# Performance work log

Hardware: AMD Instinct MI355X
Metric: run time of the kernel (lower is better)

## Reference

```python
import jax, jax.numpy as jnp
import numpy as np

N_NODES = 100000


def _degrees(src, dst, n):
    ones = jnp.ones(src.shape[0], dtype=jnp.float32)
    deg_out = jax.ops.segment_sum(ones, src, num_segments=n)
    deg_in = jax.ops.segment_sum(ones, dst, num_segments=n)
    # DGL clamps degrees to min 1 before pow(-0.5)
    return jnp.clip(deg_out, 1.0) ** -0.5, jnp.clip(deg_in, 1.0) ** -0.5


def _graph_conv(x, src, dst, W, b, norm_out, norm_in, n):
    # norm='both': scale source by D_out^-1/2, aggregate (copy_u + sum), scale dest by D_in^-1/2
    # weight applied before aggregation (in_feats >= out_feats for all layers; math-equivalent)
    h = (x * norm_out[:, None]) @ W                      # [N, out]
    agg = jax.ops.segment_sum(h[src], dst, num_segments=n)  # SpMM via gather+scatter-add
    return agg * norm_in[:, None] + b


def setup_inputs() -> dict:
    key = jax.random.key(0)
    ks = jax.random.split(key, 8)
    E = 1600000
    return {
        "in_feat": jax.random.normal(ks[0], (N_NODES, 128), dtype=jnp.float32),
        "src": jax.random.randint(ks[1], (E,), 0, N_NODES),
        "dst": jax.random.randint(ks[2], (E,), 0, N_NODES),
        "W1": jax.random.normal(ks[3], (128, 128), dtype=jnp.float32) * (128 ** -0.5),
        "b1": jnp.zeros((128,), dtype=jnp.float32),
        "W2": jax.random.normal(ks[4], (128, 128), dtype=jnp.float32) * (128 ** -0.5),
        "b2": jnp.zeros((128,), dtype=jnp.float32),
        "W3": jax.random.normal(ks[5], (128, 64), dtype=jnp.float32) * (128 ** -0.5),
        "b3": jnp.zeros((64,), dtype=jnp.float32),
    }


def reference(in_feat, src, dst, W1, b1, W2, b2, W3, b3):
    n = in_feat.shape[0]
    norm_out, norm_in = _degrees(src, dst, n)
    h = jax.nn.relu(_graph_conv(in_feat, src, dst, W1, b1, norm_out, norm_in, n))
    h = jax.nn.relu(_graph_conv(h, src, dst, W2, b2, norm_out, norm_in, n))
    h = _graph_conv(h, src, dst, W3, b3, norm_out, norm_in, n)
    return h
```

## Files before the change

kernel.cpp:

```cpp
#include <hip/hip_runtime.h>

#define THREADS 256
#define SCAN_BLK 1024
#define NR 8
#define NC 32
#define RSTRIDE 12544

typedef __attribute__((ext_vector_type(8))) short short8;
typedef __attribute__((ext_vector_type(4))) float floatx4;

__device__ __forceinline__ ushort f2bf(float f) {
    union { float f; uint u; } v; v.f = f;
    uint u = v.u;
    return (ushort)((u + 0x7FFFu + ((u >> 16) & 1u)) >> 16);
}
__device__ __forceinline__ float bf_lo(uint u) {
    union { uint u; float f; } v; v.u = u << 16; return v.f;
}
__device__ __forceinline__ float bf_hi(uint u) {
    union { uint u; float f; } v; v.u = u & 0xFFFF0000u; return v.f;
}

__global__ __launch_bounds__(256) void hist_out_kernel(const int* __restrict__ src,
                                                       int* __restrict__ cnt_out,
                                                       int n, int E) {
    __shared__ uint cnt[RSTRIDE];
    const int range = blockIdx.x % NR;
    const int chunk = blockIdx.x / NR;
    const int Rsz = (n + NR - 1) / NR;
    const int lo  = range * Rsz;
    const int R   = min(n - lo, Rsz);
    if (R <= 0) return;
    for (int i = threadIdx.x; i < R; i += THREADS) cnt[i] = 0;
    __syncthreads();
    const int per = (E + NC - 1) / NC;
    const int c0 = chunk * per;
    const int c1 = min(E, c0 + per);
    int i = c0 + threadIdx.x * 4;
    for (; i + 4 <= c1; i += THREADS * 4) {
        int4 v = *(const int4*)(src + i);
        if ((unsigned)(v.x - lo) < (unsigned)R) atomicAdd(&cnt[v.x - lo], 1u);
        if ((unsigned)(v.y - lo) < (unsigned)R) atomicAdd(&cnt[v.y - lo], 1u);
        if ((unsigned)(v.z - lo) < (unsigned)R) atomicAdd(&cnt[v.z - lo], 1u);
        if ((unsigned)(v.w - lo) < (unsigned)R) atomicAdd(&cnt[v.w - lo], 1u);
    }
    if (i < c1) {
        for (int e = i; e < c1 && e < i + 4; ++e) {
            int s = src[e];
            if ((unsigned)(s - lo) < (unsigned)R) atomicAdd(&cnt[s - lo], 1u);
        }
    }
    __syncthreads();
    for (int k = threadIdx.x; k < R; k += THREADS) {
        uint c = cnt[k];
        if (c) atomicAdd(&cnt_out[lo + k], (int)c);
    }
}

__global__ __launch_bounds__(256) void csr_phaseA(const int* __restrict__ dst,
                                                  ushort* __restrict__ PC, int n, int E) {
    __shared__ uint cnt[RSTRIDE / 2];
    const int range = blockIdx.x % NR;
    const int chunk = blockIdx.x / NR;
    const int Rsz = (n + NR - 1) / NR;
    const int lo  = range * Rsz;
    const int R   = min(n - lo, Rsz);
    if (R <= 0) return;
    const int Rp = (R + 2) >> 1;
    for (int i = threadIdx.x; i < Rp; i += THREADS) cnt[i] = 0;
    __syncthreads();
    const int per = (E + NC - 1) / NC;
    const int c0 = chunk * per;
    const int c1 = min(E, c0 + per);
    int i = c0 + threadIdx.x * 4;
    for (; i + 4 <= c1; i += THREADS * 4) {
        int4 v = *(const int4*)(dst + i);
        int kx = v.x - lo, ky = v.y - lo, kz = v.z - lo, kw = v.w - lo;
        if ((unsigned)kx < (unsigned)R) atomicAdd(&cnt[kx >> 1], (kx & 1) ? 65536u : 1u);
        if ((unsigned)ky < (unsigned)R) atomicAdd(&cnt[ky >> 1], (ky & 1) ? 65536u : 1u);
        if ((unsigned)kz < (unsigned)R) atomicAdd(&cnt[kz >> 1], (kz & 1) ? 65536u : 1u);
        if ((unsigned)kw < (unsigned)R) atomicAdd(&cnt[kw >> 1], (kw & 1) ? 65536u : 1u);
    }
    if (i < c1) {
        for (int e = i; e < c1 && e < i + 4; ++e) {
            int k = dst[e] - lo;
            if ((unsigned)k < (unsigned)R) atomicAdd(&cnt[k >> 1], (k & 1) ? 65536u : 1u);
        }
    }
    __syncthreads();
    ushort* pc = PC + (size_t)(range * NC + chunk) * RSTRIDE;
    for (int k = threadIdx.x; k < R; k += THREADS) {
        uint c = cnt[k >> 1];
        pc[k] = (ushort)((k & 1) ? (c >> 16) : (c & 0xFFFFu));
    }
}

__global__ void csr_colsum(const ushort* __restrict__ PC, int* __restrict__ cnt_in, int n) {
    int gk = blockIdx.x * blockDim.x + threadIdx.x;
    if (gk >= n) return;
    const int Rsz = (n + NR - 1) / NR;
    int r = gk / Rsz, k = gk - r * Rsz;
    int t = 0;
    #pragma unroll 4
    for (int c = 0; c < NC; ++c)
        t += PC[(size_t)(r * NC + c) * RSTRIDE + k];
    cnt_in[gk] = t;
}

__global__ void csr_mkbase(const ushort* __restrict__ PC, const int* __restrict__ row_off,
                           int* __restrict__ B, int n) {
    int gk = blockIdx.x * blockDim.x + threadIdx.x;
    if (gk >= n) return;
    const int Rsz = (n + NR - 1) / NR;
    int r = gk / Rsz, k = gk - r * Rsz;
    int base = row_off[gk];
    for (int c = 0; c < NC; ++c) {
        size_t idx = (size_t)(r * NC + c) * RSTRIDE + k;
        B[idx] = base;
        base += PC[idx];
    }
}

__global__ __launch_bounds__(256) void csr_phaseC(const int* __restrict__ src,
                                                  const int* __restrict__ dst,
                                                  const int* __restrict__ B,
                                                  int* __restrict__ csr_src, int n, int E) {
    __shared__ int cur[RSTRIDE];
    const int range = blockIdx.x % NR;
    const int chunk = blockIdx.x / NR;
    const int Rsz = (n + NR - 1) / NR;
    const int lo  = range * Rsz;
    const int R   = min(n - lo, Rsz);
    if (R <= 0) return;
    const int* b = B + (size_t)(range * NC + chunk) * RSTRIDE;
    for (int i = threadIdx.x; i < R; i += THREADS) cur[i] = b[i];
    __syncthreads();
    const int per = (E + NC - 1) / NC;
    const int c0 = chunk * per;
    const int c1 = min(E, c0 + per);
    int i = c0 + threadIdx.x * 4;
    for (; i + 4 <= c1; i += THREADS * 4) {
        int4 d = *(const int4*)(dst + i);
        int4 s = *(const int4*)(src + i);
        int kx = d.x - lo, ky = d.y - lo, kz = d.z - lo, kw = d.w - lo;
        if ((unsigned)kx < (unsigned)R) csr_src[atomicAdd(&cur[kx], 1)] = s.x;
        if ((unsigned)ky < (unsigned)R) csr_src[atomicAdd(&cur[ky], 1)] = s.y;
        if ((unsigned)kz < (unsigned)R) csr_src[atomicAdd(&cur[kz], 1)] = s.z;
        if ((unsigned)kw < (unsigned)R) csr_src[atomicAdd(&cur[kw], 1)] = s.w;
    }
    if (i < c1) {
        for (int e = i; e < c1 && e < i + 4; ++e) {
            int k = dst[e] - lo;
            if ((unsigned)k < (unsigned)R) csr_src[atomicAdd(&cur[k], 1)] = src[e];
        }
    }
}

__global__ void scan_phase1(const int* __restrict__ cnt, int* __restrict__ blk_sums, int n) {
    int base = blockIdx.x * SCAN_BLK;
    int t = threadIdx.x;
    int sum = 0;
    for (int i = t; i < SCAN_BLK; i += THREADS) {
        int idx = base + i;
        sum += (idx < n) ? cnt[idx] : 0;
    }
    __shared__ int wsum[4];
    for (int off = 32; off > 0; off >>= 1) sum += __shfl_down(sum, off);
    if ((t & 63) == 0) wsum[t >> 6] = sum;
    __syncthreads();
    if (t == 0) blk_sums[blockIdx.x] = wsum[0] + wsum[1] + wsum[2] + wsum[3];
}

__global__ void scan_phase2(int* __restrict__ blk_sums, int nb) {
    __shared__ int s[1024];
    int t = threadIdx.x;
    s[t] = (t < nb) ? blk_sums[t] : 0;
    __syncthreads();
    for (int off = 1; off < 1024; off <<= 1) {
        int v = s[t];
        if (t >= off) v += s[t - off];
        __syncthreads();
        s[t] = v;
        __syncthreads();
    }
    if (t < nb) blk_sums[t] = (t == 0) ? 0 : s[t - 1];
}

__global__ void scan_phase3(const int* __restrict__ cnt, const int* __restrict__ cnt_out,
                            const int* __restrict__ blk_sums,
                            int* __restrict__ row_off, float* __restrict__ norm_in,
                            float* __restrict__ norm_out, int n, int E) {
    __shared__ int ts[THREADS];
    int b = blockIdx.x, t = threadIdx.x;
    int base = b * SCAN_BLK + t * 4;
    int local[4], val[4]; int s = 0;
    #pragma unroll
    for (int k = 0; k < 4; ++k) {
        local[k] = s;
        int idx = base + k;
        int v = (idx < n) ? cnt[idx] : 0;
        val[k] = v;
        s += v;
    }
    ts[t] = s;
    __syncthreads();
    for (int off = 1; off < THREADS; off <<= 1) {
        int v = ts[t];
        if (t >= off) v += ts[t - off];
        __syncthreads();
        ts[t] = v;
        __syncthreads();
    }
    int excl = (t == 0) ? 0 : ts[t - 1];
    int boff = blk_sums[b];
    #pragma unroll
    for (int k = 0; k < 4; ++k) {
        int idx = base + k;
        if (idx < n) {
            row_off[idx] = boff + excl + local[k];
            norm_in[idx]  = rsqrtf((float)max(val[k], 1));
            norm_out[idx] = rsqrtf((float)max(cnt_out[idx], 1));
        }
    }
    if (b == 0 && t == 0) row_off[n] = E;
}

__device__ __forceinline__ void wpack_one(const float* __restrict__ W, ushort* __restrict__ Wpk,
                                          int OUT, int t) {
    int lane = t & 63, kk = (t >> 6) & 3, ct = t >> 8;
    int col = ct * 16 + (lane & 15);
    int k0 = kk * 32 + (lane >> 4) * 8;
    #pragma unroll
    for (int j = 0; j < 8; ++j)
        Wpk[t * 8 + j] = f2bf(W[(size_t)(k0 + j) * OUT + col]);
}

__global__ void wpack_all(const float* __restrict__ W1, const float* __restrict__ W2,
                          const float* __restrict__ W3, ushort* __restrict__ Wpk1,
                          ushort* __restrict__ Wpk2, ushort* __restrict__ Wpk3) {
    int t = blockIdx.x * blockDim.x + threadIdx.x;
    if (t < 2048)      wpack_one(W1, Wpk1, 128, t);
    else if (t < 4096) wpack_one(W2, Wpk2, 128, t - 2048);
    else if (t < 5120) wpack_one(W3, Wpk3, 64,  t - 4096);
}

template<int OUT, bool IN_F32>
__global__ __launch_bounds__(256) void mfma_gemm(const void* __restrict__ xv,
                                                 const ushort* __restrict__ Wpk,
                                                 const float* __restrict__ norm,
                                                 ushort* __restrict__ h, int n) {
    __shared__ ushort xs[64 * 136];
    const int t = threadIdx.x;
    const int row0 = blockIdx.x * 64;

    if (IN_F32) {
        const float* x = (const float*)xv;
        #pragma unroll
        for (int i = 0; i < 8; ++i) {
            int e = (i * 256 + t) * 4;
            int row = e >> 7, col = e & 127;
            int gr = min(row0 + row, n - 1);
            float nf = norm[gr];
            float4 v = *(const float4*)(x + (size_t)gr * 128 + col);
            ushort4 p;
            p.x = f2bf(v.x * nf); p.y = f2bf(v.y * nf);
            p.z = f2bf(v.z * nf); p.w = f2bf(v.w * nf);
            *(ushort4*)(&xs[row * 136 + col]) = p;
        }
    } else {
        const ushort* x = (const ushort*)xv;
        #pragma unroll
        for (int i = 0; i < 4; ++i) {
            int e = (i * 256 + t) * 8;
            int row = e >> 7, col = e & 127;
            int gr = min(row0 + row, n - 1);
            float nf = norm[gr];
            uint4 v = *(const uint4*)(x + (size_t)gr * 128 + col);
            uint4 o;
            o.x = f2bf(bf_lo(v.x) * nf) | ((uint)f2bf(bf_hi(v.x) * nf) << 16);
            o.y = f2bf(bf_lo(v.y) * nf) | ((uint)f2bf(bf_hi(v.y) * nf) << 16);
            o.z = f2bf(bf_lo(v.z) * nf) | ((uint)f2bf(bf_hi(v.z) * nf) << 16);
            o.w = f2bf(bf_lo(v.w) * nf) | ((uint)f2bf(bf_hi(v.w) * nf) << 16);
            *(uint4*)(&xs[row * 136 + col]) = o;
        }
    }
    __syncthreads();

    const int wave = t >> 6, lane = t & 63;
    const int r = lane & 15, g = lane >> 4;
    const int nrow0 = row0 + wave * 16;

    short8 a[4];
    #pragma unroll
    for (int kk = 0; kk < 4; ++kk)
        a[kk] = *(const short8*)(&xs[(wave * 16 + r) * 136 + kk * 32 + g * 8]);

    const short8* wp = (const short8*)Wpk;
    #pragma unroll
    for (int ct = 0; ct < OUT / 16; ++ct) {
        floatx4 acc = {0.f, 0.f, 0.f, 0.f};
        #pragma unroll
        for (int kk = 0; kk < 4; ++kk) {
            short8 b = wp[(ct * 4 + kk) * 64 + lane];
            acc = __builtin_amdgcn_mfma_f32_16x16x32_bf16(a[kk], b, acc, 0, 0, 0);
        }
        int col = ct * 16 + r;
        #pragma unroll
        for (int rr = 0; rr < 4; ++rr) {
            int grow = nrow0 + g * 4 + rr;
            if (grow < n) h[(size_t)grow * OUT + col] = f2bf(acc[rr]);
        }
    }
}

template<bool RELU>
__global__ __launch_bounds__(256) void agg128(const ushort* __restrict__ h,
                                              const int* __restrict__ row_off,
                                              const int* __restrict__ csr_src,
                                              const float* __restrict__ nin,
                                              const float* __restrict__ bias,
                                              ushort* __restrict__ out, int n) {
    const int wave = threadIdx.x >> 6;
    const int lane = threadIdx.x & 63;
    const uint* hu = (const uint*)h;
    for (int node = blockIdx.x * 4 + wave; node < n; node += gridDim.x * 4) {
        int beg = row_off[node], end = row_off[node + 1];
        float a0 = 0.f, a1 = 0.f;
        int j = beg;
        for (; j + 3 < end; j += 4) {
            int s0 = csr_src[j], s1 = csr_src[j + 1], s2 = csr_src[j + 2], s3 = csr_src[j + 3];
            uint u0 = hu[(size_t)s0 * 64 + lane];
            uint u1 = hu[(size_t)s1 * 64 + lane];
            uint u2 = hu[(size_t)s2 * 64 + lane];
            uint u3 = hu[(size_t)s3 * 64 + lane];
            a0 += bf_lo(u0); a1 += bf_hi(u0);
            a0 += bf_lo(u1); a1 += bf_hi(u1);
            a0 += bf_lo(u2); a1 += bf_hi(u2);
            a0 += bf_lo(u3); a1 += bf_hi(u3);
        }
        for (; j < end; ++j) {
            uint u = hu[(size_t)csr_src[j] * 64 + lane];
            a0 += bf_lo(u); a1 += bf_hi(u);
        }
        float nf = nin[node];
        float2 bb = *(const float2*)(bias + 2 * lane);
        float r0 = a0 * nf + bb.x;
        float r1 = a1 * nf + bb.y;
        if (RELU) { r0 = fmaxf(r0, 0.f); r1 = fmaxf(r1, 0.f); }
        ((uint*)out)[(size_t)node * 64 + lane] = (uint)f2bf(r0) | ((uint)f2bf(r1) << 16);
    }
}

__global__ __launch_bounds__(256) void agg64_final(const ushort* __restrict__ h,
                                                   const int* __restrict__ row_off,
                                                   const int* __restrict__ csr_src,
                                                   const float* __restrict__ nin,
                                                   const float* __restrict__ bias,
                                                   float* __restrict__ out, int n) {
    const int wave = threadIdx.x >> 6;
    const int lane = threadIdx.x & 63;
    const int half = lane >> 5, u5 = lane & 31;
    const uint* hu = (const uint*)h;
    for (int node = blockIdx.x * 4 + wave; node < n; node += gridDim.x * 4) {
        int beg = row_off[node], end = row_off[node + 1];
        float a0 = 0.f, a1 = 0.f;
        int j = beg + half;
        for (; j + 2 < end; j += 4) {
            int sA = csr_src[j], sB = csr_src[j + 2];
            uint uA = hu[(size_t)sA * 32 + u5];
            uint uB = hu[(size_t)sB * 32 + u5];
            a0 += bf_lo(uA); a1 += bf_hi(uA);
            a0 += bf_lo(uB); a1 += bf_hi(uB);
        }
        if (j < end) {
            uint u = hu[(size_t)csr_src[j] * 32 + u5];
            a0 += bf_lo(u); a1 += bf_hi(u);
        }
        float o0 = a0 + __shfl(a0, u5 + 32);
        float o1 = a1 + __shfl(a1, u5 + 32);
        if (lane < 32) {
            float nf = nin[node];
            float2 bb = *(const float2*)(bias + 2 * u5);
            float2 r;
            r.x = o0 * nf + bb.x;
            r.y = o1 * nf + bb.y;
            *(float2*)(out + (size_t)node * 64 + 2 * u5) = r;
        }
    }
}

extern "C" void kernel_launch(void* const* d_in, const int* in_sizes, int n_in,
                              void* d_out, int out_size, void* d_ws, size_t ws_size,
                              hipStream_t stream) {
    const float* in_feat = (const float*)d_in[0];
    const int*   src     = (const int*)d_in[1];
    const int*   dst     = (const int*)d_in[2];
    const float* W1      = (const float*)d_in[3];
    const float* b1      = (const float*)d_in[4];
    const float* W2      = (const float*)d_in[5];
    const float* b2      = (const float*)d_in[6];
    const float* W3      = (const float*)d_in[7];
    const float* b3      = (const float*)d_in[8];

    const int n = in_sizes[0] / 128;
    const int E = in_sizes[1];
    float* out = (float*)d_out;

    float* ws       = (float*)d_ws;
    float* norm_out = ws;
    float* norm_in  = ws + n;
    int*   row_off  = (int*)(ws + 2 * (size_t)n);
    int*   csr_src  = row_off + (n + 4);
    ushort* Wpk1    = (ushort*)(csr_src + E);
    ushort* Wpk2    = Wpk1 + 128 * 128;
    ushort* Wpk3    = Wpk2 + 128 * 128;
    ushort* bufA    = Wpk3 + 128 * 64;
    ushort* bufB    = bufA + (size_t)n * 128;
    int*    cnt_in   = (int*)bufA;
    int*    cnt_out  = cnt_in + n;
    int*    blk_sums = cnt_out + n;
    ushort* PC       = (ushort*)(blk_sums + 128);
    int*    Bbase    = (int*)(PC + (size_t)NR * NC * RSTRIDE);

    const int nb = (n + SCAN_BLK - 1) / SCAN_BLK;

    hipMemsetAsync(cnt_out, 0, (size_t)n * sizeof(int), stream);
    wpack_all<<<20, THREADS, 0, stream>>>(W1, W2, W3, Wpk1, Wpk2, Wpk3);
    hist_out_kernel<<<NR * NC, THREADS, 0, stream>>>(src, cnt_out, n, E);
    csr_phaseA<<<NR * NC, THREADS, 0, stream>>>(dst, PC, n, E);
    csr_colsum<<<(n + THREADS - 1) / THREADS, THREADS, 0, stream>>>(PC, cnt_in, n);
    scan_phase1<<<nb, THREADS, 0, stream>>>(cnt_in, blk_sums, n);
    scan_phase2<<<1, 1024, 0, stream>>>(blk_sums, nb);
    scan_phase3<<<nb, THREADS, 0, stream>>>(cnt_in, cnt_out, blk_sums, row_off, norm_in, norm_out, n, E);
    csr_mkbase<<<(n + THREADS - 1) / THREADS, THREADS, 0, stream>>>(PC, row_off, Bbase, n);
    csr_phaseC<<<NR * NC, THREADS, 0, stream>>>(src, dst, Bbase, csr_src, n, E);

    const int gemm_grid = (n + 63) / 64;
    const int agg_grid  = 4096;

    mfma_gemm<128, true><<<gemm_grid, THREADS, 0, stream>>>(in_feat, Wpk1, norm_out, bufA, n);
    agg128<true><<<agg_grid, THREADS, 0, stream>>>(bufA, row_off, csr_src, norm_in, b1, bufB, n);
    mfma_gemm<128, false><<<gemm_grid, THREADS, 0, stream>>>(bufB, Wpk2, norm_out, bufA, n);
    agg128<true><<<agg_grid, THREADS, 0, stream>>>(bufA, row_off, csr_src, norm_in, b2, bufB, n);
    mfma_gemm<64, false><<<gemm_grid, THREADS, 0, stream>>>(bufB, Wpk3, norm_out, bufA, n);
    agg64_final<<<agg_grid, THREADS, 0, stream>>>(bufA, row_off, csr_src, norm_in, b3, out, n);
}
```

Baseline: 417.4 us.

## Fuse aggregation with next-layer GEMM and switch intermediates from bf16 to fp16

The separate aggregation and GEMM kernels for layers 1→2 and 2→3 become one kernel. Each block aggregates 64 nodes into LDS, applies bias, ReLU and the out-norm, then runs the MFMA GEMM directly. This removes one intermediate write and read of the 128-wide hidden tensor per layer, plus two kernel launches. Intermediates and MFMA inputs also move from bf16 to fp16, which gives cheaper conversions but a narrower dynamic range. The fused kernel runs one block per 64 nodes with a fixed per-wave loop, which may reduce latency hiding compared with the old grid-stride aggregation.

```diff
diff --git a/kernel.cpp b/kernel.cpp
--- a/kernel.cpp
+++ b/kernel.cpp
@@ -6,19 +6,19 @@
 #define NC 32
 #define RSTRIDE 12544
 
-typedef __attribute__((ext_vector_type(8))) short short8;
+typedef __attribute__((ext_vector_type(8))) _Float16 half8;
 typedef __attribute__((ext_vector_type(4))) float floatx4;
 
-__device__ __forceinline__ ushort f2bf(float f) {
-    union { float f; uint u; } v; v.f = f;
-    uint u = v.u;
-    return (ushort)((u + 0x7FFFu + ((u >> 16) & 1u)) >> 16);
-}
-__device__ __forceinline__ float bf_lo(uint u) {
-    union { uint u; float f; } v; v.u = u << 16; return v.f;
-}
-__device__ __forceinline__ float bf_hi(uint u) {
-    union { uint u; float f; } v; v.u = u & 0xFFFF0000u; return v.f;
+__device__ __forceinline__ ushort f2h(float f) {
+    union { _Float16 h; ushort s; } v;
+    v.h = (_Float16)f;
+    return v.s;
+}
+__device__ __forceinline__ float h_lo(uint u) {
+    union { ushort s; _Float16 h; } v; v.s = (ushort)(u & 0xFFFFu); return (float)v.h;
+}
+__device__ __forceinline__ float h_hi(uint u) {
+    union { ushort s; _Float16 h; } v; v.s = (ushort)(u >> 16); return (float)v.h;
 }
 
 __global__ __launch_bounds__(256) void hist_out_kernel(const int* __restrict__ src,
@@ -232,7 +232,7 @@
     int k0 = kk * 32 + (lane >> 4) * 8;
     #pragma unroll
     for (int j = 0; j < 8; ++j)
-        Wpk[t * 8 + j] = f2bf(W[(size_t)(k0 + j) * OUT + col]);
+        Wpk[t * 8 + j] = f2h(W[(size_t)(k0 + j) * OUT + col]);
 }
 
 __global__ void wpack_all(const float* __restrict__ W1, const float* __restrict__ W2,
@@ -244,8 +244,8 @@
     else if (t < 5120) wpack_one(W3, Wpk3, 64,  t - 4096);
 }
 
-template<int OUT, bool IN_F32>
-__global__ __launch_bounds__(256) void mfma_gemm(const void* __restrict__ xv,
+template<int OUT>
+__global__ __launch_bounds__(256) void mfma_gemm(const float* __restrict__ x,
                                                  const ushort* __restrict__ Wpk,
                                                  const float* __restrict__ norm,
                                                  ushort* __restrict__ h, int n) {
@@ -253,36 +253,17 @@
     const int t = threadIdx.x;
     const int row0 = blockIdx.x * 64;
 
-    if (IN_F32) {
-        const float* x = (const float*)xv;
-        #pragma unroll
-        for (int i = 0; i < 8; ++i) {
-            int e = (i * 256 + t) * 4;
-            int row = e >> 7, col = e & 127;
-            int gr = min(row0 + row, n - 1);
-            float nf = norm[gr];
-            float4 v = *(const float4*)(x + (size_t)gr * 128 + col);
-            ushort4 p;
-            p.x = f2bf(v.x * nf); p.y = f2bf(v.y * nf);
-            p.z = f2bf(v.z * nf); p.w = f2bf(v.w * nf);
-            *(ushort4*)(&xs[row * 136 + col]) = p;
-        }
-    } else {
-        const ushort* x = (const ushort*)xv;
-        #pragma unroll
-        for (int i = 0; i < 4; ++i) {
-            int e = (i * 256 + t) * 8;
-            int row = e >> 7, col = e & 127;
-            int gr = min(row0 + row, n - 1);
-            float nf = norm[gr];
-            uint4 v = *(const uint4*)(x + (size_t)gr * 128 + col);
-            uint4 o;
-            o.x = f2bf(bf_lo(v.x) * nf) | ((uint)f2bf(bf_hi(v.x) * nf) << 16);
-            o.y = f2bf(bf_lo(v.y) * nf) | ((uint)f2bf(bf_hi(v.y) * nf) << 16);
-            o.z = f2bf(bf_lo(v.z) * nf) | ((uint)f2bf(bf_hi(v.z) * nf) << 16);
-            o.w = f2bf(bf_lo(v.w) * nf) | ((uint)f2bf(bf_hi(v.w) * nf) << 16);
-            *(uint4*)(&xs[row * 136 + col]) = o;
-        }
+    #pragma unroll
+    for (int i = 0; i < 8; ++i) {
+        int e = (i * 256 + t) * 4;
+        int row = e >> 7, col = e & 127;
+        int gr = min(row0 + row, n - 1);
+        float nf = norm[gr];
+        float4 v = *(const float4*)(x + (size_t)gr * 128 + col);
+        ushort4 p;
+        p.x = f2h(v.x * nf); p.y = f2h(v.y * nf);
+        p.z = f2h(v.z * nf); p.w = f2h(v.w * nf);
+        *(ushort4*)(&xs[row * 136 + col]) = p;
     }
     __syncthreads();
 
@@ -290,64 +271,100 @@
     const int r = lane & 15, g = lane >> 4;
     const int nrow0 = row0 + wave * 16;
 
-    short8 a[4];
+    half8 a[4];
     #pragma unroll
     for (int kk = 0; kk < 4; ++kk)
-        a[kk] = *(const short8*)(&xs[(wave * 16 + r) * 136 + kk * 32 + g * 8]);
-
-    const short8* wp = (const short8*)Wpk;
+        a[kk] = *(const half8*)(&xs[(wave * 16 + r) * 136 + kk * 32 + g * 8]);
+
+    const half8* wp = (const half8*)Wpk;
     #pragma unroll
     for (int ct = 0; ct < OUT / 16; ++ct) {
         floatx4 acc = {0.f, 0.f, 0.f, 0.f};
         #pragma unroll
         for (int kk = 0; kk < 4; ++kk) {
-            short8 b = wp[(ct * 4 + kk) * 64 + lane];
-            acc = __builtin_amdgcn_mfma_f32_16x16x32_bf16(a[kk], b, acc, 0, 0, 0);
+            half8 b = wp[(ct * 4 + kk) * 64 + lane];
+            acc = __builtin_amdgcn_mfma_f32_16x16x32_f16(a[kk], b, acc, 0, 0, 0);
         }
         int col = ct * 16 + r;
         #pragma unroll
         for (int rr = 0; rr < 4; ++rr) {
             int grow = nrow0 + g * 4 + rr;
-            if (grow < n) h[(size_t)grow * OUT + col] = f2bf(acc[rr]);
-        }
-    }
-}
-
-template<bool RELU>
-__global__ __launch_bounds__(256) void agg128(const ushort* __restrict__ h,
-                                              const int* __restrict__ row_off,
-                                              const int* __restrict__ csr_src,
-                                              const float* __restrict__ nin,
-                                              const float* __restrict__ bias,
-                                              ushort* __restrict__ out, int n) {
-    const int wave = threadIdx.x >> 6;
-    const int lane = threadIdx.x & 63;
+            if (grow < n) h[(size_t)grow * OUT + col] = f2h(acc[rr]);
+        }
+    }
+}
+
+template<int OUTN>
+__global__ __launch_bounds__(256) void fused_agg_gemm(const ushort* __restrict__ h,
+                                                      const int* __restrict__ row_off,
+                                                      const int* __restrict__ csr_src,
+                                                      const float* __restrict__ nin,
+                                                      const float* __restrict__ bias,
+                                                      const float* __restrict__ nout,
+                                                      const ushort* __restrict__ Wpk,
+                                                      ushort* __restrict__ h_next, int n) {
+    __shared__ ushort xs[64 * 136];
+    const int t = threadIdx.x;
+    const int wave = t >> 6, lane = t & 63;
+    const int row0 = blockIdx.x * 64;
     const uint* hu = (const uint*)h;
-    for (int node = blockIdx.x * 4 + wave; node < n; node += gridDim.x * 4) {
-        int beg = row_off[node], end = row_off[node + 1];
+    const float2 bb = *(const float2*)(bias + 2 * lane);
+
+    for (int i = 0; i < 16; ++i) {
+        const int lrow = wave * 16 + i;
+        const int node = row0 + lrow;
         float a0 = 0.f, a1 = 0.f;
-        int j = beg;
-        for (; j + 3 < end; j += 4) {
-            int s0 = csr_src[j], s1 = csr_src[j + 1], s2 = csr_src[j + 2], s3 = csr_src[j + 3];
-            uint u0 = hu[(size_t)s0 * 64 + lane];
-            uint u1 = hu[(size_t)s1 * 64 + lane];
-            uint u2 = hu[(size_t)s2 * 64 + lane];
-            uint u3 = hu[(size_t)s3 * 64 + lane];
-            a0 += bf_lo(u0); a1 += bf_hi(u0);
-            a0 += bf_lo(u1); a1 += bf_hi(u1);
-            a0 += bf_lo(u2); a1 += bf_hi(u2);
-            a0 += bf_lo(u3); a1 += bf_hi(u3);
-        }
-        for (; j < end; ++j) {
-            uint u = hu[(size_t)csr_src[j] * 64 + lane];
-            a0 += bf_lo(u); a1 += bf_hi(u);
-        }
-        float nf = nin[node];
-        float2 bb = *(const float2*)(bias + 2 * lane);
-        float r0 = a0 * nf + bb.x;
-        float r1 = a1 * nf + bb.y;
-        if (RELU) { r0 = fmaxf(r0, 0.f); r1 = fmaxf(r1, 0.f); }
-        ((uint*)out)[(size_t)node * 64 + lane] = (uint)f2bf(r0) | ((uint)f2bf(r1) << 16);
+        if (node < n) {
+            int beg = row_off[node], end = row_off[node + 1];
+            int j = beg;
+            for (; j + 3 < end; j += 4) {
+                int s0 = csr_src[j], s1 = csr_src[j + 1], s2 = csr_src[j + 2], s3 = csr_src[j + 3];
+                uint u0 = hu[(size_t)s0 * 64 + lane];
+                uint u1 = hu[(size_t)s1 * 64 + lane];
+                uint u2 = hu[(size_t)s2 * 64 + lane];
+                uint u3 = hu[(size_t)s3 * 64 + lane];
+                a0 += h_lo(u0); a1 += h_hi(u0);
+                a0 += h_lo(u1); a1 += h_hi(u1);
+                a0 += h_lo(u2); a1 += h_hi(u2);
+                a0 += h_lo(u3); a1 += h_hi(u3);
+            }
+            for (; j < end; ++j) {
+                uint u = hu[(size_t)csr_src[j] * 64 + lane];
+                a0 += h_lo(u); a1 += h_hi(u);
+            }
+            float nf = nin[node];
+            a0 = fmaxf(a0 * nf + bb.x, 0.f);
+            a1 = fmaxf(a1 * nf + bb.y, 0.f);
+            float no = nout[node];
+            a0 *= no; a1 *= no;
+        }
+        ((uint*)xs)[lrow * 68 + lane] = (uint)f2h(a0) | ((uint)f2h(a1) << 16);
+    }
+    __syncthreads();
+
+    const int r = lane & 15, g = lane >> 4;
+    const int nrow0 = row0 + wave * 16;
+
+    half8 a[4];
+    #pragma unroll
+    for (int kk = 0; kk < 4; ++kk)
+        a[kk] = *(const half8*)(&xs[(wave * 16 + r) * 136 + kk * 32 + g * 8]);
+
+    const half8* wp = (const half8*)Wpk;
+    #pragma unroll
+    for (int ct = 0; ct < OUTN / 16; ++ct) {
+        floatx4 acc = {0.f, 0.f, 0.f, 0.f};
+        #pragma unroll
+        for (int kk = 0; kk < 4; ++kk) {
+            half8 b = wp[(ct * 4 + kk) * 64 + lane];
+            acc = __builtin_amdgcn_mfma_f32_16x16x32_f16(a[kk], b, acc, 0, 0, 0);
+        }
+        int col = ct * 16 + r;
+        #pragma unroll
+        for (int rr = 0; rr < 4; ++rr) {
+            int grow = nrow0 + g * 4 + rr;
+            if (grow < n) h_next[(size_t)grow * OUTN + col] = f2h(acc[rr]);
+        }
     }
 }
 
@@ -369,12 +386,12 @@
             int sA = csr_src[j], sB = csr_src[j + 2];
             uint uA = hu[(size_t)sA * 32 + u5];
             uint uB = hu[(size_t)sB * 32 + u5];
-            a0 += bf_lo(uA); a1 += bf_hi(uA);
-            a0 += bf_lo(uB); a1 += bf_hi(uB);
+            a0 += h_lo(uA); a1 += h_hi(uA);
+            a0 += h_lo(uB); a1 += h_hi(uB);
         }
         if (j < end) {
             uint u = hu[(size_t)csr_src[j] * 32 + u5];
-            a0 += bf_lo(u); a1 += bf_hi(u);
+            a0 += h_lo(u); a1 += h_hi(u);
         }
         float o0 = a0 + __shfl(a0, u5 + 32);
         float o1 = a1 + __shfl(a1, u5 + 32);
@@ -435,13 +452,13 @@
     csr_mkbase<<<(n + THREADS - 1) / THREADS, THREADS, 0, stream>>>(PC, row_off, Bbase, n);
     csr_phaseC<<<NR * NC, THREADS, 0, stream>>>(src, dst, Bbase, csr_src, n, E);
 
-    const int gemm_grid = (n + 63) / 64;
+    const int tile_grid = (n + 63) / 64;
     const int agg_grid  = 4096;
 
-    mfma_gemm<128, true><<<gemm_grid, THREADS, 0, stream>>>(in_feat, Wpk1, norm_out, bufA, n);
-    agg128<true><<<agg_grid, THREADS, 0, stream>>>(bufA, row_off, csr_src, norm_in, b1, bufB, n);
-    mfma_gemm<128, false><<<gemm_grid, THREADS, 0, stream>>>(bufB, Wpk2, norm_out, bufA, n);
-    agg128<true><<<agg_grid, THREADS, 0, stream>>>(bufA, row_off, csr_src, norm_in, b2, bufB, n);
-    mfma_gemm<64, false><<<gemm_grid, THREADS, 0, stream>>>(bufB, Wpk3, norm_out, bufA, n);
+    mfma_gemm<128><<<tile_grid, THREADS, 0, stream>>>(in_feat, Wpk1, norm_out, bufA, n);
+    fused_agg_gemm<128><<<tile_grid, THREADS, 0, stream>>>(bufA, row_off, csr_src, norm_in, b1,
+                                                           norm_out, Wpk2, bufB, n);
+    fused_agg_gemm<64><<<tile_grid, THREADS, 0, stream>>>(bufB, row_off, csr_src, norm_in, b2,
+                                                          norm_out, Wpk3, bufA, n);
     agg64_final<<<agg_grid, THREADS, 0, stream>>>(bufA, row_off, csr_src, norm_in, b3, out, n);
 }
```

Measured after the change: 400.8 us. -4.0%, faster.
